# Performance work log

Hardware: AMD Instinct MI355X
Metric: run time of the kernel (lower is better)

Reference implementation:

```python
import jax, jax.numpy as jnp
import numpy as np

B, T, K, H = 8, 1024, 512, 8


def setup_inputs() -> dict:
    key = jax.random.key(0)
    kx, kq, kk, kv, ko = jax.random.split(key, 5)
    s = 0.02
    return {
        "x": jax.random.normal(kx, (B, T, K), dtype=jnp.float32),
        "Wq": jax.random.normal(kq, (K * H, K), dtype=jnp.float32) * s,
        "Wk": jax.random.normal(kk, (K * H, K), dtype=jnp.float32) * s,
        "Wv": jax.random.normal(kv, (K * H, K), dtype=jnp.float32) * s,
        "Wo": jax.random.normal(ko, (K, K * H), dtype=jnp.float32) * s,
    }


def reference(x, Wq, Wk, Wv, Wo):
    b, t, k = x.shape
    h = H
    scale = k ** 0.25  # applied to both q and k, total 1/sqrt(k)
    # torch Linear: y = x @ W.T ; view (b,t,h,k) then move heads out: (b,h,t,k)
    def proj(W):
        return (x @ W.T).reshape(b, t, h, k).transpose(0, 2, 1, 3)
    q = proj(Wq) / scale
    kk_ = proj(Wk) / scale
    v = proj(Wv)
    dot = jnp.einsum("bhtd,bhsd->bhts", q, kk_)  # (b,h,t,t)
    # causal mask: strict upper triangle (j > i) -> -inf
    causal = jnp.tril(jnp.ones((t, t), dtype=bool))
    dot = jnp.where(causal[None, None], dot, -jnp.inf)
    attn = jax.nn.softmax(dot, axis=-1)
    out = jnp.einsum("bhts,bhsd->bhtd", attn, v)  # (b,h,t,k)
    out = out.transpose(0, 2, 1, 3).reshape(b, t, h * k)
    return out @ Wo.T
```

## Files before the change

### kernel.cpp

```cpp
#include <hip/hip_runtime.h>
#include <hip/hip_bf16.h>
#include <cstdint>
#include <cmath>


typedef __attribute__((ext_vector_type(8))) short short8;
typedef __attribute__((ext_vector_type(4))) float f32x4;

#define DEVINL __device__ __forceinline__

DEVINL float bf2f(ushort u) { union { uint32_t i; float f; } w; w.i = (uint32_t)u << 16; return w.f; }
DEVINL ushort f2bf(float f) {
  union { float f; uint32_t i; } w; w.f = f;
  uint32_t r = w.i + 0x7FFFu + ((w.i >> 16) & 1u);
  return (ushort)(r >> 16);
}

DEVINL void gl_lds16(const ushort* g, ushort* l) {
  __builtin_amdgcn_global_load_lds(
      (const __attribute__((address_space(1))) uint32_t*)g,
      (__attribute__((address_space(3))) uint32_t*)l, 16, 0, 0);
}

__global__ __launch_bounds__(256) void cvt_f32_bf16(const float* __restrict__ in,
                                                    ushort* __restrict__ out,
                                                    int n8, float scale) {
  int i = blockIdx.x * 256 + threadIdx.x;
  if (i >= n8) return;
  const float4* p = (const float4*)in + (size_t)i * 2;
  float4 a = p[0], b = p[1];
  short8 o;
  o[0] = (short)f2bf(a.x * scale); o[1] = (short)f2bf(a.y * scale);
  o[2] = (short)f2bf(a.z * scale); o[3] = (short)f2bf(a.w * scale);
  o[4] = (short)f2bf(b.x * scale); o[5] = (short)f2bf(b.y * scale);
  o[6] = (short)f2bf(b.z * scale); o[7] = (short)f2bf(b.w * scale);
  ((short8*)out)[i] = o;
}

__global__ __launch_bounds__(256) void zerof4(float4* __restrict__ p, int n4) {
  int i = blockIdx.x * 256 + threadIdx.x;
  if (i < n4) p[i] = float4{0.f, 0.f, 0.f, 0.f};
}

template<bool CSKIP, bool CKB, int EPI, bool ZBH, bool SWZ>
__global__ __launch_bounds__(512, 2) void gemm256(
    const ushort* __restrict__ A0, long long sAb, long long sAh,
    const ushort* __restrict__ B0, long long sBb, long long sBh,
    void* __restrict__ C0, long long sCb, long long sCh,
    int lda, int ldb, int ldc, int K)
{
  int bm, bn;
  if (SWZ) {
    const int X = gridDim.x, nwg = X * gridDim.y;
    const int bid = blockIdx.y * X + blockIdx.x;
    const int cpx = nwg >> 3;
    const int swz = (bid & 7) * cpx + (bid >> 3);
    bm = swz % X; bn = swz / X;
  } else {
    bm = blockIdx.x; bn = blockIdx.y;
  }
  const int bz = blockIdx.z;
  if (CSKIP && bn > bm) return;
  long long za, zb, zc;
  if (ZBH) {
    const long long bi = bz >> 3, hi = bz & 7;
    za = bi * sAb + hi * sAh; zb = bi * sBb + hi * sBh; zc = bi * sCb + hi * sCh;
  } else {
    za = (long long)bz * sAh; zb = (long long)bz * sBh; zc = (long long)bz * sCh;
  }
  const ushort* A = A0 + za;
  const ushort* B = B0 + zb;
  int kend = K;
  if (CKB) { int kb = (bm + 1) * 256; kend = kb < K ? kb : K; }

  __shared__ ushort smem[65536];

  const int tid = threadIdx.x;
  const int wid = tid >> 6, lane = tid & 63;
  const int wr = wid >> 2, wc = wid & 3;
  const int l15 = lane & 15, kq = lane >> 4;

  const int srow8 = lane >> 3;
  const int schunk = ((lane & 7) ^ srow8) * 8;
  const ushort* ag = A + (size_t)(bm * 256 + wid * 8 + srow8) * lda + schunk;
  const ushort* bg = B + (size_t)(bn * 256 + wid * 8 + srow8) * ldb + schunk;

  auto STA = [&](int buf, int band, int kk) {
    gl_lds16(ag + (size_t)band * 64 * lda + kk, &smem[buf * 32768 + band * 4096 + wid * 512]);
  };
  auto STB = [&](int buf, int band, int kk) {
    gl_lds16(bg + (size_t)band * 64 * ldb + kk, &smem[buf * 32768 + 16384 + band * 4096 + wid * 512]);
  };
  auto STAGE8 = [&](int buf, int kk) {
    STB(buf, 0, kk); STB(buf, 1, kk); STB(buf, 2, kk); STB(buf, 3, kk);
    STA(buf, 0, kk); STA(buf, 2, kk); STA(buf, 1, kk); STA(buf, 3, kk);
  };

  f32x4 acc[8][4] = {};
  const int nt = kend >> 6;

  STAGE8(0, 0);

  for (int t = 0; t < nt; ++t) {
    const int cur = t & 1;
    const ushort* As = &smem[cur * 32768];
    const ushort* Bs = As + 16384;
    const bool pre = (t + 1 < nt);

    short8 bq[4], av[4];
    auto LDB = [&](int ks) {
#pragma unroll
      for (int n = 0; n < 4; ++n)
        bq[n] = *(const short8*)
            &Bs[(wc * 64 + n * 16 + l15) * 64 + (((ks * 4 + kq) ^ (l15 & 7)) * 8)];
    };
    auto LDA = [&](int mh, int ks) {
#pragma unroll
      for (int m = 0; m < 4; ++m)
        av[m] = *(const short8*)
            &As[(wr * 128 + mh * 64 + m * 16 + l15) * 64 + (((ks * 4 + kq) ^ (l15 & 7)) * 8)];
    };
    auto MFMAQ = [&](int mh) {
      __builtin_amdgcn_s_setprio(1);
#pragma unroll
      for (int m = 0; m < 4; ++m)
#pragma unroll
        for (int n = 0; n < 4; ++n)
          acc[mh * 4 + m][n] =
              __builtin_amdgcn_mfma_f32_16x16x32_bf16(av[m], bq[n], acc[mh * 4 + m][n], 0, 0, 0);
      __builtin_amdgcn_s_setprio(0);
    };

    if (pre) {
      STAGE8(cur ^ 1, (t + 1) << 6);
      asm volatile("s_waitcnt vmcnt(10)" ::: "memory");
    } else {
      asm volatile("s_waitcnt vmcnt(2)" ::: "memory");
    }
    __builtin_amdgcn_sched_barrier(0);
    __builtin_amdgcn_s_barrier();
    __builtin_amdgcn_sched_barrier(0);
    LDB(0); LDA(0, 0); MFMAQ(0);

    if (pre) asm volatile("s_waitcnt vmcnt(8)" ::: "memory");
    else     asm volatile("s_waitcnt vmcnt(0)" ::: "memory");
    __builtin_amdgcn_sched_barrier(0);
    __builtin_amdgcn_s_barrier();
    __builtin_amdgcn_sched_barrier(0);
    LDA(1, 0); MFMAQ(1);

    LDB(1); LDA(0, 1); MFMAQ(0);

    LDA(1, 1); MFMAQ(1);
    asm volatile("s_waitcnt lgkmcnt(0)" ::: "memory");
    __builtin_amdgcn_sched_barrier(0);
    __builtin_amdgcn_s_barrier();
    __builtin_amdgcn_sched_barrier(0);
  }

  if constexpr (EPI == 0) {
#pragma unroll
    for (int m = 0; m < 8; ++m)
#pragma unroll
      for (int n = 0; n < 4; ++n)
#pragma unroll
        for (int r = 0; r < 4; ++r) {
          const int row = wr * 128 + m * 16 + kq * 4 + r;
          const int col = wc * 64 + n * 16 + l15;
          smem[row * 256 + (((col >> 3) ^ (row & 31)) * 8) + (col & 7)] = f2bf(acc[m][n][r]);
        }
    __syncthreads();
    ushort* C = (ushort*)C0 + zc;
#pragma unroll
    for (int j = 0; j < 16; ++j) {
      const int chi = j * 512 + tid;
      const int row = chi >> 5, cc = chi & 31;
      *(short8*)&C[(size_t)(bm * 256 + row) * ldc + bn * 256 + cc * 8] =
          *(const short8*)&smem[row * 256 + ((cc ^ (row & 31)) * 8)];
    }
  } else {
    float* C = (float*)C0 + zc;
#pragma unroll
    for (int m = 0; m < 8; ++m)
#pragma unroll
      for (int n = 0; n < 4; ++n)
#pragma unroll
        for (int r = 0; r < 4; ++r)
          atomicAdd(&C[(size_t)(bm * 256 + wr * 128 + m * 16 + kq * 4 + r) * ldc
                       + bn * 256 + wc * 64 + n * 16 + l15], acc[m][n][r]);
  }
}

__global__ __launch_bounds__(256) void transposeV(const ushort* __restrict__ QKVg,
                                                  ushort* __restrict__ Vtg) {
  __shared__ ushort tile[64][72];
  const int bx = blockIdx.x;
  const int by = blockIdx.y;
  const int bz = blockIdx.z;
  const int b = bz >> 3, h = bz & 7;
  const int t = threadIdx.x;
  const int r = t >> 2, c = (t & 3) * 16;

  const ushort* src = QKVg + (size_t)(b * 1024 + bx * 64 + r) * 12288 + 8192 + h * 512 + by * 64 + c;
  short8 v0 = *(const short8*)src;
  short8 v1 = *(const short8*)(src + 8);
#pragma unroll
  for (int j = 0; j < 8; ++j) { tile[r][c + j] = (ushort)v0[j]; tile[r][c + 8 + j] = (ushort)v1[j]; }
  __syncthreads();

  ushort* dst = Vtg + (size_t)(bz * 512 + by * 64 + r) * 1024 + bx * 64 + c;
  short8 o0, o1;
#pragma unroll
  for (int j = 0; j < 8; ++j) { o0[j] = (short)tile[c + j][r]; o1[j] = (short)tile[c + 8 + j][r]; }
  *(short8*)dst = o0;
  *(short8*)(dst + 8) = o1;
}

__global__ __launch_bounds__(256) void softmax_causal(ushort* __restrict__ S) {
  const int wave = threadIdx.x >> 6, lane = threadIdx.x & 63;
  const size_t row_id = (size_t)blockIdx.x * 4 + wave;
  const int t = (int)(row_id & 1023);
  ushort* row = S + row_id * 1024;
  const int j0 = lane * 16;

  short8 v0 = *(const short8*)&row[j0];
  short8 v1 = *(const short8*)&row[j0 + 8];
  float f[16];
#pragma unroll
  for (int i = 0; i < 8; ++i) { f[i] = bf2f((ushort)v0[i]); f[8 + i] = bf2f((ushort)v1[i]); }

  float m = -1e30f;
#pragma unroll
  for (int i = 0; i < 16; ++i) {
    if (j0 + i > t) f[i] = -1e30f;
    m = fmaxf(m, f[i]);
  }
#pragma unroll
  for (int off = 32; off; off >>= 1) m = fmaxf(m, __shfl_xor(m, off));

  float s = 0.f;
#pragma unroll
  for (int i = 0; i < 16; ++i) { f[i] = __expf(f[i] - m); s += f[i]; }
#pragma unroll
  for (int off = 32; off; off >>= 1) s += __shfl_xor(s, off);
  const float inv = 1.f / s;

#pragma unroll
  for (int i = 0; i < 8; ++i) {
    v0[i] = (short)f2bf(f[i] * inv);
    v1[i] = (short)f2bf(f[8 + i] * inv);
  }
  *(short8*)&row[j0] = v0;
  *(short8*)&row[j0 + 8] = v1;
}

extern "C" void kernel_launch(void* const* d_in, const int* in_sizes, int n_in,
                              void* d_out, int out_size, void* d_ws, size_t ws_size,
                              hipStream_t stream) {
  const float* x  = (const float*)d_in[0];
  const float* Wq = (const float*)d_in[1];
  const float* Wk = (const float*)d_in[2];
  const float* Wv = (const float*)d_in[3];
  const float* Wo = (const float*)d_in[4];
  float* out = (float*)d_out;

  const int g = (ws_size >= 293601280ull) ? 4 : (ws_size >= 192937984ull) ? 2 : 1;
  const int ng = 8 / g;

  ushort* xb   = (ushort*)d_ws;
  ushort* Wqkv = xb   + (size_t)4194304;
  ushort* Wob  = Wqkv + (size_t)6291456;
  ushort* AO   = Wob  + (size_t)2097152;
  ushort* QKVg = AO   + (size_t)33554432;
  ushort* Vtg  = QKVg + (size_t)g * 12582912;
  ushort* Sg   = Vtg  + (size_t)g * 4194304;

  const float iscale = (float)(1.0 / pow(512.0, 0.25));

  cvt_f32_bf16<<<2048, 256, 0, stream>>>(x,  xb,             524288, 1.0f);
  cvt_f32_bf16<<<1024, 256, 0, stream>>>(Wq, Wqkv,           262144, iscale);
  cvt_f32_bf16<<<1024, 256, 0, stream>>>(Wk, Wqkv + 2097152, 262144, iscale);
  cvt_f32_bf16<<<1024, 256, 0, stream>>>(Wv, Wqkv + 4194304, 262144, 1.0f);
  cvt_f32_bf16<<<1024, 256, 0, stream>>>(Wo, Wob,            262144, 1.0f);

  for (int grp = 0; grp < ng; ++grp) {
    gemm256<false, false, 0, false, true><<<dim3(g * 4, 48, 1), 512, 0, stream>>>(
        xb + (size_t)grp * g * 524288, 0, 0,
        Wqkv, 0, 0,
        QKVg, 0, 0,
        512, 512, 12288, 512);

    transposeV<<<dim3(16, 8, 8 * g), 256, 0, stream>>>(QKVg, Vtg);

    gemm256<true, false, 0, true, false><<<dim3(4, 4, 8 * g), 512, 0, stream>>>(
        QKVg,        12582912LL, 512LL,
        QKVg + 4096, 12582912LL, 512LL,
        Sg,          8388608LL,  1048576LL,
        12288, 12288, 1024, 512);

    softmax_causal<<<g * 2048, 256, 0, stream>>>(Sg);

    gemm256<false, true, 0, true, false><<<dim3(4, 2, 8 * g), 512, 0, stream>>>(
        Sg,  8388608LL, 1048576LL,
        Vtg, 4194304LL, 524288LL,
        AO + (size_t)grp * g * 4194304, 4194304LL, 512LL,
        1024, 1024, 4096, 1024);
  }

  zerof4<<<4096, 256, 0, stream>>>((float4*)out, 1048576);
  gemm256<false, false, 2, false, false><<<dim3(32, 2, 4), 512, 0, stream>>>(
      AO,  0, 1024LL,
      Wob, 0, 1024LL,
      out, 0, 0LL,
      4096, 4096, 512, 1024);
}
```

Baseline: 598.1 us.

## Replace QK^T/softmax/PV kernels with fused flash-attention kernel with causal block skipping

Replaces the separate score GEMM, full-row softmax and PV GEMM with a single flash-attention style kernel that keeps scores on chip, uses online softmax, and only iterates over causal KV tiles. K and V tiles are double-buffered into LDS via direct global-to-LDS loads. The V projection is written temporarily into the AO buffer and transposed from there, which frees the score buffer so more batches can be processed per group. This removes the large bf16 score-matrix round trips and the computation of masked upper-triangle blocks. In exchange it adds per-tile synchronisation and high register use for the 32 output accumulators per wave, and it relies on a last template flag being flipped on the output GEMM.

```diff
diff --git a/kernel.cpp b/kernel.cpp
--- a/kernel.cpp
+++ b/kernel.cpp
@@ -191,8 +191,173 @@
   }
 }
 
-__global__ __launch_bounds__(256) void transposeV(const ushort* __restrict__ QKVg,
-                                                  ushort* __restrict__ Vtg) {
+__global__ __launch_bounds__(512) void fused_attn(
+    const ushort* __restrict__ QKg, const ushort* __restrict__ Vtg,
+    ushort* __restrict__ AOg)
+{
+  const int qb = blockIdx.x;
+  const int bh = blockIdx.y;
+  const int b = bh >> 3, h = bh & 7;
+
+  __shared__ ushort smem[69632];
+
+  const int tid = threadIdx.x;
+  const int wid = tid >> 6, lane = tid & 63;
+  const int l15 = lane & 15, kq = lane >> 4;
+
+  const ushort* Qb = QKg + (size_t)(b * 1024 + qb * 128 + wid * 16) * 8192 + h * 512;
+  const ushort* Kb = QKg + (size_t)b * 1024 * 8192 + 4096 + h * 512;
+  const ushort* Vb = Vtg + (size_t)bh * 524288;
+
+  short8 qf[16];
+#pragma unroll
+  for (int kt = 0; kt < 16; ++kt)
+    qf[kt] = *(const short8*)&Qb[(size_t)l15 * 8192 + kt * 32 + kq * 8];
+
+  auto STAGE = [&](int buf, int t) {
+    const int s0 = t * 32;
+#pragma unroll
+    for (int q = 0; q < 4; ++q) {
+      const int r = wid * 4 + q;
+      const int sc = (lane & 56) | ((lane ^ r) & 7);
+      gl_lds16(Kb + (size_t)(s0 + r) * 8192 + sc * 8, &smem[buf * 32768 + r * 512]);
+    }
+#pragma unroll
+    for (int q = 0; q < 4; ++q) {
+      const int dbase = wid * 64 + q * 16;
+      const int d = dbase + (lane >> 2);
+      const int sc = ((lane & 3) ^ ((lane >> 2) & 3)) * 8;
+      gl_lds16(Vb + (size_t)d * 1024 + s0 + sc, &smem[buf * 32768 + 16384 + dbase * 32]);
+    }
+  };
+
+  const int nkv = (qb + 1) * 4;
+  const int qrow0 = qb * 128 + wid * 16 + kq * 4;
+  float mrow[4] = {-3e38f, -3e38f, -3e38f, -3e38f};
+  float lrow[4] = {0.f, 0.f, 0.f, 0.f};
+  f32x4 accO[32] = {};
+  ushort* PS = &smem[65536 + wid * 512];
+
+  STAGE(0, 0);
+  for (int t = 0; t < nkv; ++t) {
+    const int cur = t & 1;
+    if (t + 1 < nkv) {
+      STAGE(cur ^ 1, t + 1);
+      asm volatile("s_waitcnt vmcnt(8)" ::: "memory");
+    } else {
+      asm volatile("s_waitcnt vmcnt(0)" ::: "memory");
+    }
+    __builtin_amdgcn_sched_barrier(0);
+    __builtin_amdgcn_s_barrier();
+    __builtin_amdgcn_sched_barrier(0);
+
+    const ushort* KL = &smem[cur * 32768];
+    const ushort* VL = KL + 16384;
+    const int s0 = t * 32;
+
+    f32x4 sA = {0.f, 0.f, 0.f, 0.f}, sB = {0.f, 0.f, 0.f, 0.f};
+    __builtin_amdgcn_s_setprio(1);
+#pragma unroll
+    for (int kt = 0; kt < 16; ++kt) {
+      const int gc = kt * 4 + kq;
+      const int pos = ((gc & 56) | ((gc ^ l15) & 7)) * 8;
+      short8 k0 = *(const short8*)&KL[l15 * 512 + pos];
+      short8 k1 = *(const short8*)&KL[(16 + l15) * 512 + pos];
+      sA = __builtin_amdgcn_mfma_f32_16x16x32_bf16(qf[kt], k0, sA, 0, 0, 0);
+      sB = __builtin_amdgcn_mfma_f32_16x16x32_bf16(qf[kt], k1, sB, 0, 0, 0);
+    }
+    __builtin_amdgcn_s_setprio(0);
+
+    float p0[4], p1[4], rmax[4];
+    int nogrow = 1;
+#pragma unroll
+    for (int r = 0; r < 4; ++r) {
+      float a = sA[r], c = sB[r];
+      if (s0 + l15      > qrow0 + r) a = -3e38f;
+      if (s0 + 16 + l15 > qrow0 + r) c = -3e38f;
+      p0[r] = a; p1[r] = c;
+      float mx = fmaxf(a, c);
+      mx = fmaxf(mx, __shfl_xor(mx, 1));
+      mx = fmaxf(mx, __shfl_xor(mx, 2));
+      mx = fmaxf(mx, __shfl_xor(mx, 4));
+      mx = fmaxf(mx, __shfl_xor(mx, 8));
+      rmax[r] = mx;
+      nogrow = nogrow && (mx <= mrow[r]);
+    }
+    if (__all(nogrow)) {
+#pragma unroll
+      for (int r = 0; r < 4; ++r) {
+        p0[r] = __expf(p0[r] - mrow[r]);
+        p1[r] = __expf(p1[r] - mrow[r]);
+        float s = p0[r] + p1[r];
+        s += __shfl_xor(s, 1); s += __shfl_xor(s, 2);
+        s += __shfl_xor(s, 4); s += __shfl_xor(s, 8);
+        lrow[r] += s;
+      }
+    } else {
+#pragma unroll
+      for (int r = 0; r < 4; ++r) {
+        float mn = fmaxf(mrow[r], rmax[r]);
+        float sc = __expf(mrow[r] - mn);
+        mrow[r] = mn;
+        p0[r] = __expf(p0[r] - mn);
+        p1[r] = __expf(p1[r] - mn);
+        float s = p0[r] + p1[r];
+        s += __shfl_xor(s, 1); s += __shfl_xor(s, 2);
+        s += __shfl_xor(s, 4); s += __shfl_xor(s, 8);
+        lrow[r] = lrow[r] * sc + s;
+#pragma unroll
+        for (int j = 0; j < 32; ++j) accO[j][r] *= sc;
+      }
+    }
+
+#pragma unroll
+    for (int r = 0; r < 4; ++r) {
+      const int q = kq * 4 + r;
+      const int s1 = 16 + l15;
+      PS[q * 32 + (((l15 >> 3) ^ (q & 3)) * 8) + (l15 & 7)] = f2bf(p0[r]);
+      PS[q * 32 + (((s1 >> 3) ^ (q & 3)) * 8) + (s1 & 7)]   = f2bf(p1[r]);
+    }
+    short8 pa = *(const short8*)&PS[l15 * 32 + ((kq ^ (l15 & 3)) * 8)];
+
+    __builtin_amdgcn_s_setprio(1);
+#pragma unroll
+    for (int j = 0; j < 32; ++j) {
+      short8 bv = *(const short8*)&VL[(j * 16 + l15) * 32 + ((kq ^ (l15 & 3)) * 8)];
+      accO[j] = __builtin_amdgcn_mfma_f32_16x16x32_bf16(pa, bv, accO[j], 0, 0, 0);
+    }
+    __builtin_amdgcn_s_setprio(0);
+
+    asm volatile("s_waitcnt lgkmcnt(0)" ::: "memory");
+    __builtin_amdgcn_sched_barrier(0);
+    __builtin_amdgcn_s_barrier();
+    __builtin_amdgcn_sched_barrier(0);
+  }
+
+  float inv[4];
+#pragma unroll
+  for (int r = 0; r < 4; ++r) inv[r] = 1.f / lrow[r];
+  ushort* OS = &smem[wid * 8192];
+#pragma unroll
+  for (int j = 0; j < 32; ++j)
+#pragma unroll
+    for (int r = 0; r < 4; ++r) {
+      const int q = kq * 4 + r;
+      const int col = j * 16 + l15;
+      const int ch = col >> 3;
+      OS[q * 512 + (((ch & 56) | ((ch ^ q) & 7)) * 8) + (col & 7)] = f2bf(accO[j][r] * inv[r]);
+    }
+  ushort* AOb = AOg + (size_t)(b * 1024 + qb * 128 + wid * 16) * 4096 + h * 512;
+#pragma unroll
+  for (int it = 0; it < 16; ++it) {
+    const int q = it, c = lane;
+    const int pos = (c & 56) | ((c ^ q) & 7);
+    *(short8*)&AOb[(size_t)q * 4096 + c * 8] = *(const short8*)&OS[q * 512 + pos * 8];
+  }
+}
+
+__global__ __launch_bounds__(256) void transposeV(const ushort* __restrict__ Vtmp,
+                                                  ushort* __restrict__ Vt) {
   __shared__ ushort tile[64][72];
   const int bx = blockIdx.x;
   const int by = blockIdx.y;
@@ -201,57 +366,19 @@
   const int t = threadIdx.x;
   const int r = t >> 2, c = (t & 3) * 16;
 
-  const ushort* src = QKVg + (size_t)(b * 1024 + bx * 64 + r) * 12288 + 8192 + h * 512 + by * 64 + c;
+  const ushort* src = Vtmp + (size_t)(b * 1024 + bx * 64 + r) * 4096 + h * 512 + by * 64 + c;
   short8 v0 = *(const short8*)src;
   short8 v1 = *(const short8*)(src + 8);
 #pragma unroll
   for (int j = 0; j < 8; ++j) { tile[r][c + j] = (ushort)v0[j]; tile[r][c + 8 + j] = (ushort)v1[j]; }
   __syncthreads();
 
-  ushort* dst = Vtg + (size_t)(bz * 512 + by * 64 + r) * 1024 + bx * 64 + c;
+  ushort* dst = Vt + (size_t)(bz * 512 + by * 64 + r) * 1024 + bx * 64 + c;
   short8 o0, o1;
 #pragma unroll
   for (int j = 0; j < 8; ++j) { o0[j] = (short)tile[c + j][r]; o1[j] = (short)tile[c + 8 + j][r]; }
   *(short8*)dst = o0;
   *(short8*)(dst + 8) = o1;
-}
-
-__global__ __launch_bounds__(256) void softmax_causal(ushort* __restrict__ S) {
-  const int wave = threadIdx.x >> 6, lane = threadIdx.x & 63;
-  const size_t row_id = (size_t)blockIdx.x * 4 + wave;
-  const int t = (int)(row_id & 1023);
-  ushort* row = S + row_id * 1024;
-  const int j0 = lane * 16;
-
-  short8 v0 = *(const short8*)&row[j0];
-  short8 v1 = *(const short8*)&row[j0 + 8];
-  float f[16];
-#pragma unroll
-  for (int i = 0; i < 8; ++i) { f[i] = bf2f((ushort)v0[i]); f[8 + i] = bf2f((ushort)v1[i]); }
-
-  float m = -1e30f;
-#pragma unroll
-  for (int i = 0; i < 16; ++i) {
-    if (j0 + i > t) f[i] = -1e30f;
-    m = fmaxf(m, f[i]);
-  }
-#pragma unroll
-  for (int off = 32; off; off >>= 1) m = fmaxf(m, __shfl_xor(m, off));
-
-  float s = 0.f;
-#pragma unroll
-  for (int i = 0; i < 16; ++i) { f[i] = __expf(f[i] - m); s += f[i]; }
-#pragma unroll
-  for (int off = 32; off; off >>= 1) s += __shfl_xor(s, off);
-  const float inv = 1.f / s;
-
-#pragma unroll
-  for (int i = 0; i < 8; ++i) {
-    v0[i] = (short)f2bf(f[i] * inv);
-    v1[i] = (short)f2bf(f[8 + i] * inv);
-  }
-  *(short8*)&row[j0] = v0;
-  *(short8*)&row[j0 + 8] = v1;
 }
 
 extern "C" void kernel_launch(void* const* d_in, const int* in_sizes, int n_in,
@@ -264,16 +391,15 @@
   const float* Wo = (const float*)d_in[4];
   float* out = (float*)d_out;
 
-  const int g = (ws_size >= 293601280ull) ? 4 : (ws_size >= 192937984ull) ? 2 : 1;
+  const int g = (ws_size >= 293601280ull) ? 8 : (ws_size >= 192937984ull) ? 4 : 2;
   const int ng = 8 / g;
 
   ushort* xb   = (ushort*)d_ws;
   ushort* Wqkv = xb   + (size_t)4194304;
   ushort* Wob  = Wqkv + (size_t)6291456;
   ushort* AO   = Wob  + (size_t)2097152;
-  ushort* QKVg = AO   + (size_t)33554432;
-  ushort* Vtg  = QKVg + (size_t)g * 12582912;
-  ushort* Sg   = Vtg  + (size_t)g * 4194304;
+  ushort* QKg  = AO   + (size_t)33554432;
+  ushort* Vtg  = QKg  + (size_t)g * 8388608;
 
   const float iscale = (float)(1.0 / pow(512.0, 0.25));
 
@@ -284,31 +410,22 @@
   cvt_f32_bf16<<<1024, 256, 0, stream>>>(Wo, Wob,            262144, 1.0f);
 
   for (int grp = 0; grp < ng; ++grp) {
-    gemm256<false, false, 0, false, true><<<dim3(g * 4, 48, 1), 512, 0, stream>>>(
-        xb + (size_t)grp * g * 524288, 0, 0,
-        Wqkv, 0, 0,
-        QKVg, 0, 0,
-        512, 512, 12288, 512);
-
-    transposeV<<<dim3(16, 8, 8 * g), 256, 0, stream>>>(QKVg, Vtg);
-
-    gemm256<true, false, 0, true, false><<<dim3(4, 4, 8 * g), 512, 0, stream>>>(
-        QKVg,        12582912LL, 512LL,
-        QKVg + 4096, 12582912LL, 512LL,
-        Sg,          8388608LL,  1048576LL,
-        12288, 12288, 1024, 512);
-
-    softmax_causal<<<g * 2048, 256, 0, stream>>>(Sg);
-
-    gemm256<false, true, 0, true, false><<<dim3(4, 2, 8 * g), 512, 0, stream>>>(
-        Sg,  8388608LL, 1048576LL,
-        Vtg, 4194304LL, 524288LL,
-        AO + (size_t)grp * g * 4194304, 4194304LL, 512LL,
-        1024, 1024, 4096, 1024);
+    const ushort* xg = xb + (size_t)grp * g * 524288;
+    ushort* AOg = AO + (size_t)grp * g * 4194304;
+
+    gemm256<false, false, 0, false, true><<<dim3(g * 4, 32, 1), 512, 0, stream>>>(
+        xg, 0, 0, Wqkv, 0, 0, QKg, 0, 0, 512, 512, 8192, 512);
+
+    gemm256<false, false, 0, false, true><<<dim3(g * 4, 16, 1), 512, 0, stream>>>(
+        xg, 0, 0, Wqkv + 4194304, 0, 0, AOg, 0, 0, 512, 512, 4096, 512);
+
+    transposeV<<<dim3(16, 8, 8 * g), 256, 0, stream>>>(AOg, Vtg);
+
+    fused_attn<<<dim3(8, 8 * g), 512, 0, stream>>>(QKg, Vtg, AOg);
   }
 
   zerof4<<<4096, 256, 0, stream>>>((float4*)out, 1048576);
-  gemm256<false, false, 2, false, false><<<dim3(32, 2, 4), 512, 0, stream>>>(
+  gemm256<false, false, 2, false, true><<<dim3(32, 2, 4), 512, 0, stream>>>(
       AO,  0, 1024LL,
       Wob, 0, 1024LL,
       out, 0, 0LL,
```

After: 1.593 ms. 166% more time.
